# Optimization experiments

Measured on AMD Instinct MI355X. Metric: run time of the kernel, lower is better.

Reference implementation:

```python
import jax, jax.numpy as jnp
import numpy as np

WIDE = 15
PAD = (WIDE - 1) // 2
FREQS = np.array([1., 2., 3., 4., 5., 6.], dtype=np.float32)  # wave_base_ml frequencies


def _lstm_dir(x, wih, whh, b):
    # x: [B,T,F]; wih: [4H,F]; whh: [4H,H]; b: [4H] (b_ih+b_hh fused)
    H = whh.shape[1]
    xg = jnp.einsum('btf,gf->btg', x, wih) + b  # precompute input projections
    def step(carry, xt):
        h, c = carry
        g = xt + h @ whh.T
        i, f, gg, o = jnp.split(g, 4, axis=-1)  # torch gate order i,f,g,o
        c = jax.nn.sigmoid(f) * c + jax.nn.sigmoid(i) * jnp.tanh(gg)
        h = jax.nn.sigmoid(o) * jnp.tanh(c)
        return (h, c), h
    h0 = jnp.zeros((x.shape[0], H), x.dtype)
    _, hs = jax.lax.scan(step, (h0, h0), jnp.swapaxes(xg, 0, 1))
    return jnp.swapaxes(hs, 0, 1)


def _bn(x, g, b, eps=1e-5):
    # training-mode BatchNorm1d over (N, L) per channel; x: [B,C,L]
    m = jnp.mean(x, axis=(0, 2), keepdims=True)
    v = jnp.var(x, axis=(0, 2), keepdims=True)
    return (x - m) * jax.lax.rsqrt(v + eps) * g[None, :, None] + b[None, :, None]


def _conv1d(x, w, b):
    y = jax.lax.conv_general_dilated(x, w, (1,), 'VALID', dimension_numbers=('NCH', 'OIH', 'NCH'))
    return y + b[None, :, None]


def _haar(x):
    s = 0.7071067811865476
    return (x[..., ::2] + x[..., 1::2]) * s, (x[..., ::2] - x[..., 1::2]) * s


def _forward(x, lstm_wif, lstm_whf, lstm_bf, lstm_wir, lstm_whr, lstm_br, base_w, base_b,
             g1, be1, g2, be2, g3, be3, g4, be4, g5, be5,
             w2, b2, w3, b3, w4, b4, w5, b5, fcw, fcb):
    xt = jnp.swapaxes(x, 1, 2)  # [B,T,F]
    fwd = _lstm_dir(xt, lstm_wif, lstm_whf, lstm_bf)
    bwd = _lstm_dir(xt[:, ::-1], lstm_wir, lstm_whr, lstm_br)[:, ::-1]
    X = jnp.swapaxes(jnp.concatenate([fwd, bwd], axis=-1), 1, 2)  # [B,C,T], C=2*dim
    B, C, T = X.shape
    Xp = jnp.pad(X, ((0, 0), (0, 0), (PAD, PAD)))
    # shared sliding windows [B,C,T,WIDE] used both for scale conv and Furi_conv
    Xwin = jnp.stack([Xp[..., k:k + T] for k in range(WIDE)], axis=-1)
    offs = (jnp.arange(WIDE, dtype=X.dtype) - PAD) / WIDE
    outs = []
    for ii in range(len(FREQS)):
        scales = jax.nn.relu(jnp.einsum('bctk,k->bct', Xwin, base_w[ii]) + base_b[ii])
        # per-position cosine Fourier basis generated from the learned scales
        bases = jnp.cos((2.0 * np.pi * FREQS[ii]) * scales[..., None] * offs)  # [B,C,T,WIDE]
        o = jnp.sum(Xwin * bases, axis=-1)  # position-dependent (dynamic) conv
        sqrs = jnp.sqrt((jnp.trunc(scales * WIDE) + 1.0) / (WIDE + 2) * 2.0)
        outs.append(o / sqrs)
    wave = jnp.stack(outs, axis=1).reshape(B, -1, T)  # [B, n_waves*C, T] (wave-major, matches torch cat+view)
    out = _bn(wave, g1, be1)
    out = _bn(jax.nn.relu(_conv1d(out, w2, b2)), g2, be2)
    out = _bn(jax.nn.relu(_conv1d(out, w3, b3)), g3, be3)
    out_back = out  # [B, V_dim, L3]
    out = _bn(jax.nn.relu(_conv1d(out, w4, b4)), g4, be4)  # [B,16,L3-2]
    # 4-level Haar DWT; 5 subbands upsampled to L3, averaged over channels
    a1, d1 = _haar(out_back); a2, d2 = _haar(a1); a3, d3 = _haar(a2); a4, d4 = _haar(a3)
    L3 = out_back.shape[-1]
    bands = [jnp.repeat(bb, L3 // bb.shape[-1], axis=-1) for bb in (a4, d4, d3, d2, d1)]
    dwt = jnp.stack([bb.mean(axis=1) for bb in bands], axis=1)  # [B,5,L3]
    odwt = _bn(jax.nn.relu(_conv1d(dwt, w5, b5)), g5, be5)  # [B,16,L3-2]
    out = jnp.concatenate([out, odwt], axis=-1)
    out = out.mean(axis=-1)  # AdaptiveAvgPool1d(1) + squeeze
    return out @ fcw.T + fcb


def setup_inputs() -> dict:
    key = jax.random.key(0)
    ks = iter(jax.random.split(key, 40))
    def p(shape, s=0.05):
        return jax.random.normal(next(ks), shape, jnp.float32) * s
    B, F, T, DIM, NW, Vd = 32, 64, 518, 64, 6, 32
    C = 2 * DIM
    return {
        'x': jax.random.normal(next(ks), (B, F, T), jnp.float32),
        'lstm_wif': p((4 * DIM, F)), 'lstm_whf': p((4 * DIM, DIM)), 'lstm_bf': p((4 * DIM,)),
        'lstm_wir': p((4 * DIM, F)), 'lstm_whr': p((4 * DIM, DIM)), 'lstm_br': p((4 * DIM,)),
        'base_w': p((NW, WIDE)), 'base_b': p((NW,)),
        'g1': jnp.ones((C * NW,)), 'be1': jnp.zeros((C * NW,)),
        'g2': jnp.ones((128,)), 'be2': jnp.zeros((128,)),
        'g3': jnp.ones((Vd,)), 'be3': jnp.zeros((Vd,)),
        'g4': jnp.ones((16,)), 'be4': jnp.zeros((16,)),
        'g5': jnp.ones((16,)), 'be5': jnp.zeros((16,)),
        'w2': p((128, C * NW, 3)), 'b2': p((128,)),
        'w3': p((Vd, 128, 5)), 'b3': p((Vd,)),
        'w4': p((16, Vd, 3)), 'b4': p((16,)),
        'w5': p((16, 5, 3)), 'b5': p((16,)),
        'fcw': p((10, 16)), 'fcb': p((10,)),
    }


def reference(x, lstm_wif, lstm_whf, lstm_bf, lstm_wir, lstm_whr, lstm_br, base_w, base_b,
              g1, be1, g2, be2, g3, be3, g4, be4, g5, be5,
              w2, b2, w3, b3, w4, b4, w5, b5, fcw, fcb):
    return _forward(x, lstm_wif, lstm_whf, lstm_bf, lstm_wir, lstm_whr, lstm_br, base_w, base_b,
                    g1, be1, g2, be2, g3, be3, g4, be4, g5, be5,
                    w2, b2, w3, b3, w4, b4, w5, b5, fcw, fcb)
```

## Files before the change

### kernel.cpp

```cpp
#include <hip/hip_runtime.h>
#include <math.h>

#define B_     32
#define F_     64
#define T_     518
#define HID    64
#define GATES  256
#define CCH    128
#define NWAVE  6
#define WCH    768
#define L2_    516
#define L3_    512
#define L4_    510

__device__ __forceinline__ float frcp(float x) { return __builtin_amdgcn_rcpf(x); }
__device__ __forceinline__ float fsigmoid(float x) { return frcp(1.f + __expf(-x)); }
__device__ __forceinline__ float ftanh(float x) { return 1.f - 2.f * frcp(1.f + __expf(2.f * x)); }

__global__ void xg_kernel(const float* __restrict__ x,
                          const float* __restrict__ wif, const float* __restrict__ bf,
                          const float* __restrict__ wir, const float* __restrict__ br,
                          float* __restrict__ xg_f, float* __restrict__ xg_r,
                          float* __restrict__ stats) {
    if (blockIdx.x == 0 && blockIdx.y == 0) {
        for (int i = threadIdx.x; i < 2 * WCH; i += 256) stats[i] = 0.f;
    }
    const int tid = threadIdx.x;
    const int wv  = tid >> 7;
    const int g2  = tid & 1;
    const int r   = (tid >> 1) & 63;
    const int g   = (2 * wv + g2) * 64 + r;
    const int b   = blockIdx.y;
    const int t0  = blockIdx.x * 8;
    float4 wa[16], wb[16];
    const float4* w0 = (const float4*)(wif + g * F_);
    const float4* w1 = (const float4*)(wir + g * F_);
#pragma unroll
    for (int i = 0; i < 16; ++i) { wa[i] = w0[i]; wb[i] = w1[i]; }
    const float bfv = bf[g], brv = br[g];
    for (int tt = 0; tt < 8; ++tt) {
        const int t = t0 + tt;
        if (t >= T_) break;
        const float* xp = x + (size_t)b * F_ * T_ + t;
        float a0 = bfv, a1 = brv;
#pragma unroll
        for (int i = 0; i < 16; ++i) {
            float x0 = xp[(i * 4 + 0) * T_];
            float x1 = xp[(i * 4 + 1) * T_];
            float x2 = xp[(i * 4 + 2) * T_];
            float x3 = xp[(i * 4 + 3) * T_];
            a0 += wa[i].x * x0 + wa[i].y * x1 + wa[i].z * x2 + wa[i].w * x3;
            a1 += wb[i].x * x0 + wb[i].y * x1 + wb[i].z * x2 + wb[i].w * x3;
        }
        const size_t o = ((size_t)b * T_ + t) * GATES + tid;
        xg_f[o] = a0;
        xg_r[o] = a1;
    }
}

__global__ __launch_bounds__(128, 1) void lstm_kernel(
        const float* __restrict__ xgi_f, const float* __restrict__ xgi_r,
        const float* __restrict__ whf, const float* __restrict__ whr,
        float* __restrict__ X) {
    const int dir = blockIdx.x & 1;
    const int b   = blockIdx.x >> 1;
    const float* xg  = (dir ? xgi_r : xgi_f) + (size_t)b * T_ * GATES;
    const float* whh = dir ? whr : whf;
    const int tid = threadIdx.x;
    const int r   = tid & 63;
    const int w   = tid >> 6;

    float4 wA[16], wB[16];
    {
        const float4* pA = (const float4*)(whh + (size_t)((2 * w) * HID + r) * HID);
        const float4* pB = (const float4*)(whh + (size_t)((2 * w + 1) * HID + r) * HID);
#pragma unroll
        for (int i = 0; i < 16; ++i) { wA[i] = pA[i]; wB[i] = pB[i]; }
    }

    __shared__ __align__(16) float hs[2][HID];
    __shared__ __align__(16) float gbuf[2][HID][4];
    hs[w][r] = 0.f;
    float c = 0.f;
    float* Xrow = X + ((size_t)(b * CCH + dir * HID + r)) * T_;

    int t = dir ? (T_ - 1) : 0;
    const int step = dir ? -1 : 1;
    const float2* xg2 = (const float2*)xg;
    float2 q0 = xg2[((size_t)t * 2 + w) * 64 + r];
    float2 q1 = xg2[((size_t)(t + step) * 2 + w) * 64 + r];

    for (int s = 0; s < T_; ++s) {
        float4 a0 = {q0.x, 0.f, 0.f, 0.f};
        float4 a1 = {q0.y, 0.f, 0.f, 0.f};
        const float4* h4p = (const float4*)hs[w];
#pragma unroll
        for (int i = 0; i < 16; ++i) {
            const float4 h4 = h4p[i];
            a0.x = fmaf(wA[i].x, h4.x, a0.x); a0.y = fmaf(wA[i].y, h4.y, a0.y);
            a0.z = fmaf(wA[i].z, h4.z, a0.z); a0.w = fmaf(wA[i].w, h4.w, a0.w);
            a1.x = fmaf(wB[i].x, h4.x, a1.x); a1.y = fmaf(wB[i].y, h4.y, a1.y);
            a1.z = fmaf(wB[i].z, h4.z, a1.z); a1.w = fmaf(wB[i].w, h4.w, a1.w);
        }
        const float gA = (a0.x + a0.y) + (a0.z + a0.w);
        const float gB = (a1.x + a1.y) + (a1.z + a1.w);
        const int buf = s & 1;
        *(float2*)&gbuf[buf][r][2 * w] = make_float2(gA, gB);

        int tp = t + 2 * step;
        tp = tp < 0 ? 0 : (tp >= T_ ? T_ - 1 : tp);
        const float2 qn = xg2[((size_t)tp * 2 + w) * 64 + r];

        asm volatile("s_waitcnt lgkmcnt(0)" ::: "memory");
        __builtin_amdgcn_s_barrier();

        const float4 g4 = *(const float4*)gbuf[buf][r];
        const float si = fsigmoid(g4.x);
        const float sf = fsigmoid(g4.y);
        const float so = fsigmoid(g4.w);
        c = sf * c + si * ftanh(g4.z);
        const float h = so * ftanh(c);

        hs[w][r] = h;
        if (w == 0) Xrow[t] = h;
        q0 = q1; q1 = qn;
        t += step;
    }
}

__global__ void wave_kernel(const float* __restrict__ X,
                            const float* __restrict__ bw, const float* __restrict__ bb,
                            float* __restrict__ wave, float* __restrict__ stats) {
    const int b = blockIdx.z, c = blockIdx.y;
    const int t0 = blockIdx.x * 256;
    const int tid = threadIdx.x;
    __shared__ float xs[256 + 14];
    __shared__ float bws[NWAVE][16];
    __shared__ float bbs[NWAVE];
    __shared__ float red[4][12];
    const float* xrow = X + ((size_t)(b * CCH + c)) * T_;
    for (int i = tid; i < 270; i += 256) {
        int tt = t0 - 7 + i;
        xs[i] = (tt >= 0 && tt < T_) ? xrow[tt] : 0.f;
    }
    if (tid < NWAVE * 15) bws[tid / 15][tid % 15] = bw[tid];
    if (tid < NWAVE) bbs[tid] = bb[tid];
    __syncthreads();
    const int t = t0 + tid;
    float ls[NWAVE], lq[NWAVE];
#pragma unroll
    for (int ii = 0; ii < NWAVE; ++ii) { ls[ii] = 0.f; lq[ii] = 0.f; }
    if (t < T_) {
        float win[15];
#pragma unroll
        for (int k = 0; k < 15; ++k) win[k] = xs[tid + k];
        float e[8];
        e[0] = win[7];
#pragma unroll
        for (int m = 1; m < 8; ++m) e[m] = win[7 - m] + win[7 + m];
        const float c0 = 6.28318530717958647692f / 15.f;
#pragma unroll
        for (int ii = 0; ii < NWAVE; ++ii) {
            float sc = bbs[ii];
#pragma unroll
            for (int k = 0; k < 15; ++k) sc += win[k] * bws[ii][k];
            sc = fmaxf(sc, 0.f);
            const float phi = c0 * (float)(ii + 1) * sc;
            float o = e[0];
#pragma unroll
            for (int m = 1; m < 8; ++m) o += e[m] * __cosf(phi * (float)m);
            const float q = (truncf(sc * 15.f) + 1.f) * (2.f / 17.f);
            const float val = o * rsqrtf(q);
            wave[((size_t)(b * WCH + ii * CCH + c)) * T_ + t] = val;
            ls[ii] = val;
            lq[ii] = val * val;
        }
    }
#pragma unroll
    for (int off = 32; off > 0; off >>= 1) {
#pragma unroll
        for (int ii = 0; ii < NWAVE; ++ii) {
            ls[ii] += __shfl_down(ls[ii], off);
            lq[ii] += __shfl_down(lq[ii], off);
        }
    }
    if ((tid & 63) == 0) {
        const int w = tid >> 6;
#pragma unroll
        for (int ii = 0; ii < NWAVE; ++ii) { red[w][ii] = ls[ii]; red[w][6 + ii] = lq[ii]; }
    }
    __syncthreads();
    if (tid < 12) {
        const float a = red[0][tid] + red[1][tid] + red[2][tid] + red[3][tid];
        const int ii = tid % 6;
        const int ch = ii * CCH + c;
        atomicAdd(&stats[(tid >= 6 ? WCH : 0) + ch], a);
    }
}

__global__ void bn1_finalize_kernel(const float* __restrict__ stats,
                                    float* __restrict__ mean, float* __restrict__ rstd) {
    const int c = threadIdx.x;
    const float n = (float)(B_ * T_);
    const float m = stats[c] / n;
    const float v = stats[WCH + c] / n - m * m;
    mean[c] = m;
    rstd[c] = rsqrtf(v + 1e-5f);
}

__global__ void bn_stats_kernel(const float* __restrict__ x, int Bn, int C, int L,
                                float* __restrict__ mean, float* __restrict__ rstd) {
    const int c = blockIdx.x;
    const int tid = threadIdx.x;
    float s = 0.f, s2 = 0.f;
    for (int b = 0; b < Bn; ++b) {
        const float* row = x + ((size_t)b * C + c) * L;
        for (int l = tid; l < L; l += 256) { float v = row[l]; s += v; s2 += v * v; }
    }
#pragma unroll
    for (int off = 32; off > 0; off >>= 1) { s += __shfl_down(s, off); s2 += __shfl_down(s2, off); }
    __shared__ float ss[4], ss2[4];
    if ((tid & 63) == 0) { ss[tid >> 6] = s; ss2[tid >> 6] = s2; }
    __syncthreads();
    if (tid == 0) {
        float S = ss[0] + ss[1] + ss[2] + ss[3];
        float S2 = ss2[0] + ss2[1] + ss2[2] + ss2[3];
        float n = (float)(Bn * L);
        float m = S / n;
        float v = S2 / n - m * m;
        mean[c] = m;
        rstd[c] = rsqrtf(v + 1e-5f);
    }
}

__global__ void bnfold2_kernel(const float* __restrict__ w2, const float* __restrict__ b2,
                               const float* __restrict__ m1, const float* __restrict__ r1,
                               const float* __restrict__ g1, const float* __restrict__ be1,
                               float* __restrict__ w2t, float* __restrict__ b2t) {
    const int o = blockIdx.x, tid = threadIdx.x;
    float part = 0.f;
    for (int idx = tid; idx < WCH * 3; idx += 256) {
        const int c = idx / 3;
        const float sc = r1[c] * g1[c];
        const float sh = be1[c] - m1[c] * sc;
        const float wv = w2[(size_t)o * (WCH * 3) + idx];
        w2t[(size_t)idx * 128 + o] = wv * sc;
        part += wv * sh;
    }
#pragma unroll
    for (int off = 32; off > 0; off >>= 1) part += __shfl_down(part, off);
    __shared__ float red[4];
    if ((tid & 63) == 0) red[tid >> 6] = part;
    __syncthreads();
    if (tid == 0) b2t[o] = b2[o] + red[0] + red[1] + red[2] + red[3];
}

__global__ void bnfold3_kernel(const float* __restrict__ w3, const float* __restrict__ b3,
                               const float* __restrict__ m2, const float* __restrict__ r2,
                               const float* __restrict__ g2, const float* __restrict__ be2,
                               float* __restrict__ w3t, float* __restrict__ b3t) {
    const int o = blockIdx.x, tid = threadIdx.x;
    float part = 0.f;
    for (int idx = tid; idx < 128 * 5; idx += 256) {
        const int c = idx / 5;
        const float sc = r2[c] * g2[c];
        const float sh = be2[c] - m2[c] * sc;
        const float wv = w3[(size_t)o * 640 + idx];
        w3t[(size_t)idx * 32 + o] = wv * sc;
        part += wv * sh;
    }
#pragma unroll
    for (int off = 32; off > 0; off >>= 1) part += __shfl_down(part, off);
    __shared__ float red[4];
    if ((tid & 63) == 0) red[tid >> 6] = part;
    __syncthreads();
    if (tid == 0) b3t[o] = b3[o] + red[0] + red[1] + red[2] + red[3];
}

__global__ void bnfold4_kernel(const float* __restrict__ w4, const float* __restrict__ b4,
                               const float* __restrict__ m3, const float* __restrict__ r3,
                               const float* __restrict__ g3, const float* __restrict__ be3,
                               float* __restrict__ w4t, float* __restrict__ b4t,
                               float* __restrict__ bnp3) {
    const int o = blockIdx.x, tid = threadIdx.x;
    float part = 0.f;
    if (tid < 96) {
        const int c = tid / 3;
        const float sc = r3[c] * g3[c];
        const float sh = be3[c] - m3[c] * sc;
        const float wv = w4[(size_t)o * 96 + tid];
        w4t[(size_t)tid * 16 + o] = wv * sc;
        part = wv * sh;
    }
    if (o == 0 && tid >= 96) {
        const int ch = tid - 96;
        const float sc = r3[ch] * g3[ch];
        bnp3[ch] = sc;
        bnp3[32 + ch] = be3[ch] - m3[ch] * sc;
    }
#pragma unroll
    for (int off = 32; off > 0; off >>= 1) part += __shfl_down(part, off);
    __shared__ float red[2];
    if ((tid & 63) == 0) red[tid >> 6] = part;
    __syncthreads();
    if (tid == 0) b4t[o] = b4[o] + red[0] + red[1];
}

__global__ __launch_bounds__(256) void conv2_kernel(
        const float* __restrict__ in, const float* __restrict__ wt,
        const float* __restrict__ bt, float* __restrict__ out) {
    const int b  = blockIdx.x;
    const int t  = blockIdx.y * 256 + threadIdx.x;
    const int o0 = blockIdx.z * 16;
    if (t >= L2_) return;
    float acc[16];
#pragma unroll
    for (int j = 0; j < 16; ++j) acc[j] = bt[o0 + j];
    const float* inb = in + (size_t)b * WCH * T_ + t;
    for (int c = 0; c < WCH; ++c) {
        const float x0 = inb[c * T_], x1 = inb[c * T_ + 1], x2 = inb[c * T_ + 2];
        const float* wc = wt + (size_t)c * 384 + o0;
#pragma unroll
        for (int j = 0; j < 16; ++j)
            acc[j] = fmaf(x0, wc[j], fmaf(x1, wc[128 + j], fmaf(x2, wc[256 + j], acc[j])));
    }
    const size_t ob = ((size_t)b * 128 + o0) * L2_ + t;
#pragma unroll
    for (int j = 0; j < 16; ++j) out[ob + (size_t)j * L2_] = fmaxf(acc[j], 0.f);
}

__global__ __launch_bounds__(256) void conv3_kernel(
        const float* __restrict__ in, const float* __restrict__ wt,
        const float* __restrict__ bt, float* __restrict__ out) {
    const int b  = blockIdx.x;
    const int t  = blockIdx.y * 256 + threadIdx.x;
    const int o0 = blockIdx.z * 8;
    float acc[8];
#pragma unroll
    for (int j = 0; j < 8; ++j) acc[j] = bt[o0 + j];
    const float* inb = in + (size_t)b * 128 * L2_ + t;
    for (int c = 0; c < 128; ++c) {
        const float x0 = inb[c * L2_], x1 = inb[c * L2_ + 1], x2 = inb[c * L2_ + 2];
        const float x3 = inb[c * L2_ + 3], x4 = inb[c * L2_ + 4];
        const float* wc = wt + (size_t)c * 160 + o0;
#pragma unroll
        for (int j = 0; j < 8; ++j) {
            float a = fmaf(x0, wc[j], acc[j]);
            a = fmaf(x1, wc[32 + j], a);
            a = fmaf(x2, wc[64 + j], a);
            a = fmaf(x3, wc[96 + j], a);
            acc[j] = fmaf(x4, wc[128 + j], a);
        }
    }
    const size_t ob = ((size_t)b * 32 + o0) * L3_ + t;
#pragma unroll
    for (int j = 0; j < 8; ++j) out[ob + (size_t)j * L3_] = fmaxf(acc[j], 0.f);
}

__global__ __launch_bounds__(256) void conv4_kernel(
        const float* __restrict__ in, const float* __restrict__ wt,
        const float* __restrict__ bt, float* __restrict__ out) {
    const int b = blockIdx.x;
    const int t = blockIdx.y * 256 + threadIdx.x;
    if (t >= L4_) return;
    float acc[16];
#pragma unroll
    for (int j = 0; j < 16; ++j) acc[j] = bt[j];
    const float* inb = in + (size_t)b * 32 * L3_ + t;
    for (int c = 0; c < 32; ++c) {
        const float x0 = inb[c * L3_], x1 = inb[c * L3_ + 1], x2 = inb[c * L3_ + 2];
        const float* wc = wt + (size_t)c * 48;
#pragma unroll
        for (int j = 0; j < 16; ++j)
            acc[j] = fmaf(x0, wc[j], fmaf(x1, wc[16 + j], fmaf(x2, wc[32 + j], acc[j])));
    }
    const size_t ob = ((size_t)b * 16) * L4_ + t;
#pragma unroll
    for (int j = 0; j < 16; ++j) out[ob + (size_t)j * L4_] = fmaxf(acc[j], 0.f);
}

__global__ __launch_bounds__(512) void dwt_conv5_kernel(const float* __restrict__ y3,
                                                        const float* __restrict__ w5,
                                                        const float* __restrict__ b5,
                                                        const float* __restrict__ bnp3,
                                                        float* __restrict__ y5) {
    const int b = blockIdx.x, l = threadIdx.x;
    __shared__ float cm[L3_];
    __shared__ float bands[5][L3_];
    __shared__ float w5s[240];
    __shared__ float b5s[16];
    __shared__ float sc3s[32], sh3s[32];
    if (l < 240) w5s[l] = w5[l];
    if (l < 16) b5s[l] = b5[l];
    if (l >= 256 && l < 288) sc3s[l - 256] = bnp3[l - 256];
    if (l >= 288 && l < 320) sh3s[l - 288] = bnp3[32 + (l - 288)];
    __syncthreads();
    float s = 0.f, shs = 0.f;
    for (int ch = 0; ch < 32; ++ch) {
        s = fmaf(y3[((size_t)b * 32 + ch) * L3_ + l], sc3s[ch], s);
        shs += sh3s[ch];
    }
    cm[l] = (s + shs) * (1.f / 32.f);
    __syncthreads();
    const float s1 = 0.70710678118654752440f;
    const float s2c = 0.5f;
    const float s3 = 0.35355339059327378f;
    const float s4 = 0.25f;
    const int b16 = l & ~15, b8 = l & ~7, b4v = l & ~3, b2v = l & ~1;
    float sa = 0.f, sb = 0.f;
#pragma unroll
    for (int i = 0; i < 8; ++i) { sa += cm[b16 + i]; sb += cm[b16 + 8 + i]; }
    bands[0][l] = (sa + sb) * s4;
    bands[1][l] = (sa - sb) * s4;
    float ta = 0.f, tb = 0.f;
#pragma unroll
    for (int i = 0; i < 4; ++i) { ta += cm[b8 + i]; tb += cm[b8 + 4 + i]; }
    bands[2][l] = (ta - tb) * s3;
    bands[3][l] = (cm[b4v] + cm[b4v + 1] - cm[b4v + 2] - cm[b4v + 3]) * s2c;
    bands[4][l] = (cm[b2v] - cm[b2v + 1]) * s1;
    __syncthreads();
    if (l < L4_) {
        float in3[5][3];
#pragma unroll
        for (int c = 0; c < 5; ++c) {
            in3[c][0] = bands[c][l]; in3[c][1] = bands[c][l + 1]; in3[c][2] = bands[c][l + 2];
        }
#pragma unroll
        for (int o = 0; o < 16; ++o) {
            float acc = b5s[o];
#pragma unroll
            for (int c = 0; c < 5; ++c) {
                const float* wp = &w5s[(o * 5 + c) * 3];
                acc += in3[c][0] * wp[0] + in3[c][1] * wp[1] + in3[c][2] * wp[2];
            }
            y5[((size_t)b * 16 + o) * L4_ + l] = fmaxf(acc, 0.f);
        }
    }
}

__global__ __launch_bounds__(512) void tail_final_kernel(
        const float* __restrict__ y4, const float* __restrict__ y5,
        const float* __restrict__ g4, const float* __restrict__ be4,
        const float* __restrict__ g5, const float* __restrict__ be5,
        const float* __restrict__ fcw, const float* __restrict__ fcb,
        float* __restrict__ out) {
    const int p = threadIdx.x;
    const int b = p >> 4, ch = p & 15;
    const float2* p4 = (const float2*)(y4 + ((size_t)(b * 16 + ch)) * L4_);
    const float2* p5 = (const float2*)(y5 + ((size_t)(b * 16 + ch)) * L4_);
    float s4 = 0.f, q4 = 0.f, s5 = 0.f, q5 = 0.f;
    for (int i = 0; i < L4_ / 2; ++i) {
        float2 a = p4[i], bb2 = p5[i];
        s4 += a.x + a.y;  q4 += a.x * a.x + a.y * a.y;
        s5 += bb2.x + bb2.y; q5 += bb2.x * bb2.x + bb2.y * bb2.y;
    }
    __shared__ float S4[512], Q4[512], S5[512], Q5[512];
    __shared__ float M4[16], R4[16], M5[16], R5[16];
    __shared__ float pool[B_][16];
    S4[p] = s4; Q4[p] = q4; S5[p] = s5; Q5[p] = q5;
    __syncthreads();
    if (p < 16) {
        float ts = 0.f, tq = 0.f, us = 0.f, uq = 0.f;
        for (int bb = 0; bb < B_; ++bb) {
            ts += S4[bb * 16 + p]; tq += Q4[bb * 16 + p];
            us += S5[bb * 16 + p]; uq += Q5[bb * 16 + p];
        }
        const float n = (float)(B_ * L4_);
        float m = ts / n; M4[p] = m; R4[p] = rsqrtf(tq / n - m * m + 1e-5f);
        m = us / n;       M5[p] = m; R5[p] = rsqrtf(uq / n - m * m + 1e-5f);
    }
    __syncthreads();
    {
        const float mm4 = s4 / (float)L4_, mm5 = s5 / (float)L4_;
        const float v4 = (mm4 - M4[ch]) * R4[ch] * g4[ch] + be4[ch];
        const float v5 = (mm5 - M5[ch]) * R5[ch] * g5[ch] + be5[ch];
        pool[b][ch] = 0.5f * (v4 + v5);
    }
    __syncthreads();
    if (p < B_ * 10) {
        const int bb = p / 10, row = p - bb * 10;
        float a = fcb[row];
#pragma unroll
        for (int c = 0; c < 16; ++c) a += pool[bb][c] * fcw[row * 16 + c];
        out[bb * 10 + row] = a;
    }
}

extern "C" void kernel_launch(void* const* d_in, const int* in_sizes, int n_in,
                              void* d_out, int out_size, void* d_ws, size_t ws_size,
                              hipStream_t stream) {
    (void)in_sizes; (void)n_in; (void)out_size; (void)ws_size;
    const float* x   = (const float*)d_in[0];
    const float* wif = (const float*)d_in[1];
    const float* whf = (const float*)d_in[2];
    const float* bf  = (const float*)d_in[3];
    const float* wir = (const float*)d_in[4];
    const float* whr = (const float*)d_in[5];
    const float* br  = (const float*)d_in[6];
    const float* bw  = (const float*)d_in[7];
    const float* bb  = (const float*)d_in[8];
    const float* g1  = (const float*)d_in[9];  const float* be1 = (const float*)d_in[10];
    const float* g2  = (const float*)d_in[11]; const float* be2 = (const float*)d_in[12];
    const float* g3  = (const float*)d_in[13]; const float* be3 = (const float*)d_in[14];
    const float* g4  = (const float*)d_in[15]; const float* be4 = (const float*)d_in[16];
    const float* g5  = (const float*)d_in[17]; const float* be5 = (const float*)d_in[18];
    const float* w2  = (const float*)d_in[19]; const float* b2  = (const float*)d_in[20];
    const float* w3  = (const float*)d_in[21]; const float* b3  = (const float*)d_in[22];
    const float* w4  = (const float*)d_in[23]; const float* b4  = (const float*)d_in[24];
    const float* w5  = (const float*)d_in[25]; const float* b5  = (const float*)d_in[26];
    const float* fcw = (const float*)d_in[27]; const float* fcb = (const float*)d_in[28];
    float* out = (float*)d_out;
    float* ws  = (float*)d_ws;

    float* xg_f  = ws;
    float* xg_r  = ws + 4243456;
    float* wave  = ws;
    float* X     = ws + 12730368;
    float* y2    = ws + 14852096;
    float* y3    = ws + 16965632;
    float* y4    = ws + 17489920;
    float* y5    = ws + 17751040;
    float* stats = ws + 18012160;
    float* m1 = ws + 18013696; float* r1 = m1 + 768;
    float* m2 = r1 + 768;      float* r2 = m2 + 128;
    float* m3 = r2 + 128;      float* r3 = m3 + 32;
    float* w2t  = X;
    float* b2t  = X + 294912;
    float* w3t  = X + 295040;
    float* b3t  = X + 315520;
    float* w4t  = X + 315552;
    float* b4t  = X + 317088;
    float* bnp3 = X + 317104;

    xg_kernel<<<dim3(65, 32), 256, 0, stream>>>(x, wif, bf, wir, br, xg_f, xg_r, stats);
    lstm_kernel<<<dim3(64), 128, 0, stream>>>(xg_f, xg_r, whf, whr, X);
    wave_kernel<<<dim3(3, CCH, B_), 256, 0, stream>>>(X, bw, bb, wave, stats);
    bn1_finalize_kernel<<<dim3(1), 768, 0, stream>>>(stats, m1, r1);
    bnfold2_kernel<<<dim3(128), 256, 0, stream>>>(w2, b2, m1, r1, g1, be1, w2t, b2t);
    conv2_kernel<<<dim3(32, 3, 8), 256, 0, stream>>>(wave, w2t, b2t, y2);
    bn_stats_kernel<<<dim3(128), 256, 0, stream>>>(y2, B_, 128, L2_, m2, r2);
    bnfold3_kernel<<<dim3(32), 256, 0, stream>>>(w3, b3, m2, r2, g2, be2, w3t, b3t);
    conv3_kernel<<<dim3(32, 2, 4), 256, 0, stream>>>(y2, w3t, b3t, y3);
    bn_stats_kernel<<<dim3(32), 256, 0, stream>>>(y3, B_, 32, L3_, m3, r3);
    bnfold4_kernel<<<dim3(16), 128, 0, stream>>>(w4, b4, m3, r3, g3, be3, w4t, b4t, bnp3);
    conv4_kernel<<<dim3(32, 2), 256, 0, stream>>>(y3, w4t, b4t, y4);
    dwt_conv5_kernel<<<dim3(B_), 512, 0, stream>>>(y3, w5, b5, bnp3, y5);
    tail_final_kernel<<<dim3(1), 512, 0, stream>>>(y4, y5, g4, be4, g5, be5, fcw, fcb, out);
}
```

Measured before the change: 1.023 ms.

## Split LSTM recurrence across 256 threads, one gate row per thread

The LSTM kernel now runs 256 threads per block, each owning one gate row of the recurrent weight matrix held in 64 registers (pinned with empty asm). Previously 128 threads each handled two gate rows. This halves the serial per-step matvec chain per thread and changes the xg layout to a plain gate-major order, which the xg kernel now writes directly. In exchange every step pays a four-wave __syncthreads instead of a two-wave barrier, and more waves run the redundant elementwise gate math.

Result: slower. 1.082 ms (+5.8%).

```diff
diff --git a/kernel.cpp b/kernel.cpp
--- a/kernel.cpp
+++ b/kernel.cpp
@@ -17,6 +17,10 @@
 __device__ __forceinline__ float fsigmoid(float x) { return frcp(1.f + __expf(-x)); }
 __device__ __forceinline__ float ftanh(float x) { return 1.f - 2.f * frcp(1.f + __expf(2.f * x)); }
 
+#define PIN8(a0,a1,a2,a3,a4,a5,a6,a7) \
+    asm volatile("" : "+v"(a0), "+v"(a1), "+v"(a2), "+v"(a3), \
+                      "+v"(a4), "+v"(a5), "+v"(a6), "+v"(a7))
+
 __global__ void xg_kernel(const float* __restrict__ x,
                           const float* __restrict__ wif, const float* __restrict__ bf,
                           const float* __restrict__ wir, const float* __restrict__ br,
@@ -26,10 +30,7 @@
         for (int i = threadIdx.x; i < 2 * WCH; i += 256) stats[i] = 0.f;
     }
     const int tid = threadIdx.x;
-    const int wv  = tid >> 7;
-    const int g2  = tid & 1;
-    const int r   = (tid >> 1) & 63;
-    const int g   = (2 * wv + g2) * 64 + r;
+    const int g   = tid;
     const int b   = blockIdx.y;
     const int t0  = blockIdx.x * 8;
     float4 wa[16], wb[16];
@@ -58,7 +59,7 @@
     }
 }
 
-__global__ __launch_bounds__(128, 1) void lstm_kernel(
+__global__ __launch_bounds__(256, 1) void lstm_kernel(
         const float* __restrict__ xgi_f, const float* __restrict__ xgi_r,
         const float* __restrict__ whf, const float* __restrict__ whr,
         float* __restrict__ X) {
@@ -70,55 +71,60 @@
     const int r   = tid & 63;
     const int w   = tid >> 6;
 
-    float4 wA[16], wB[16];
+    float wreg[64];
     {
-        const float4* pA = (const float4*)(whh + (size_t)((2 * w) * HID + r) * HID);
-        const float4* pB = (const float4*)(whh + (size_t)((2 * w + 1) * HID + r) * HID);
-#pragma unroll
-        for (int i = 0; i < 16; ++i) { wA[i] = pA[i]; wB[i] = pB[i]; }
-    }
-
-    __shared__ __align__(16) float hs[2][HID];
-    __shared__ __align__(16) float gbuf[2][HID][4];
+        const float4* p = (const float4*)(whh + (size_t)(w * HID + r) * HID);
+#pragma unroll
+        for (int i = 0; i < 16; ++i) {
+            const float4 v = p[i];
+            wreg[4 * i] = v.x; wreg[4 * i + 1] = v.y;
+            wreg[4 * i + 2] = v.z; wreg[4 * i + 3] = v.w;
+        }
+    }
+#pragma unroll
+    for (int i = 0; i < 64; i += 8)
+        PIN8(wreg[i], wreg[i + 1], wreg[i + 2], wreg[i + 3],
+             wreg[i + 4], wreg[i + 5], wreg[i + 6], wreg[i + 7]);
+
+    __shared__ __align__(16) float hs[4][HID];
+    __shared__ float gbuf[2][4][HID];
     hs[w][r] = 0.f;
     float c = 0.f;
     float* Xrow = X + ((size_t)(b * CCH + dir * HID + r)) * T_;
 
     int t = dir ? (T_ - 1) : 0;
     const int step = dir ? -1 : 1;
-    const float2* xg2 = (const float2*)xg;
-    float2 q0 = xg2[((size_t)t * 2 + w) * 64 + r];
-    float2 q1 = xg2[((size_t)(t + step) * 2 + w) * 64 + r];
+    float q0 = xg[(size_t)t * GATES + tid];
+    float q1 = xg[(size_t)(t + step) * GATES + tid];
 
     for (int s = 0; s < T_; ++s) {
-        float4 a0 = {q0.x, 0.f, 0.f, 0.f};
-        float4 a1 = {q0.y, 0.f, 0.f, 0.f};
+        float a0 = q0, a1 = 0.f, a2 = 0.f, a3 = 0.f;
         const float4* h4p = (const float4*)hs[w];
 #pragma unroll
         for (int i = 0; i < 16; ++i) {
             const float4 h4 = h4p[i];
-            a0.x = fmaf(wA[i].x, h4.x, a0.x); a0.y = fmaf(wA[i].y, h4.y, a0.y);
-            a0.z = fmaf(wA[i].z, h4.z, a0.z); a0.w = fmaf(wA[i].w, h4.w, a0.w);
-            a1.x = fmaf(wB[i].x, h4.x, a1.x); a1.y = fmaf(wB[i].y, h4.y, a1.y);
-            a1.z = fmaf(wB[i].z, h4.z, a1.z); a1.w = fmaf(wB[i].w, h4.w, a1.w);
-        }
-        const float gA = (a0.x + a0.y) + (a0.z + a0.w);
-        const float gB = (a1.x + a1.y) + (a1.z + a1.w);
+            a0 = fmaf(wreg[4 * i], h4.x, a0);
+            a1 = fmaf(wreg[4 * i + 1], h4.y, a1);
+            a2 = fmaf(wreg[4 * i + 2], h4.z, a2);
+            a3 = fmaf(wreg[4 * i + 3], h4.w, a3);
+        }
         const int buf = s & 1;
-        *(float2*)&gbuf[buf][r][2 * w] = make_float2(gA, gB);
+        gbuf[buf][w][r] = (a0 + a1) + (a2 + a3);
 
         int tp = t + 2 * step;
         tp = tp < 0 ? 0 : (tp >= T_ ? T_ - 1 : tp);
-        const float2 qn = xg2[((size_t)tp * 2 + w) * 64 + r];
-
-        asm volatile("s_waitcnt lgkmcnt(0)" ::: "memory");
-        __builtin_amdgcn_s_barrier();
-
-        const float4 g4 = *(const float4*)gbuf[buf][r];
-        const float si = fsigmoid(g4.x);
-        const float sf = fsigmoid(g4.y);
-        const float so = fsigmoid(g4.w);
-        c = sf * c + si * ftanh(g4.z);
+        const float qn = xg[(size_t)tp * GATES + tid];
+
+        __syncthreads();
+
+        const float gi = gbuf[buf][0][r];
+        const float gf = gbuf[buf][1][r];
+        const float gg = gbuf[buf][2][r];
+        const float go = gbuf[buf][3][r];
+        const float si = fsigmoid(gi);
+        const float sf = fsigmoid(gf);
+        const float so = fsigmoid(go);
+        c = sf * c + si * ftanh(gg);
         const float h = so * ftanh(c);
 
         hs[w][r] = h;
@@ -533,7 +539,7 @@
     float* bnp3 = X + 317104;
 
     xg_kernel<<<dim3(65, 32), 256, 0, stream>>>(x, wif, bf, wir, br, xg_f, xg_r, stats);
-    lstm_kernel<<<dim3(64), 128, 0, stream>>>(xg_f, xg_r, whf, whr, X);
+    lstm_kernel<<<dim3(64), 256, 0, stream>>>(xg_f, xg_r, whf, whr, X);
     wave_kernel<<<dim3(3, CCH, B_), 256, 0, stream>>>(X, bw, bb, wave, stats);
     bn1_finalize_kernel<<<dim3(1), 768, 0, stream>>>(stats, m1, r1);
     bnfold2_kernel<<<dim3(128), 256, 0, stream>>>(w2, b2, m1, r1, g1, be1, w2t, b2t);
```
